# Kernel tuning notes

Measured on AMD Instinct MI355X. Metric: run time of the kernel, lower is better.

The kernel has to match this reference:

```python
import jax, jax.numpy as jnp
import numpy as np

# Model dims (mamba_ssm defaults: expand=2, d_state=16, d_conv=4, dt_rank=ceil(d_model/16))
V, D_MODEL, N_LAYERS = 32000, 768, 2
D_INNER, D_STATE, D_CONV, DT_RANK = 1536, 16, 4, 48
BATCH, SEQ = 2, 2048


def setup_inputs() -> dict:
    key = jax.random.key(0)
    ks = jax.random.split(key, 10)

    def nrm(k, shape, s=0.02):
        return (jax.random.normal(k, shape) * s).astype(jnp.float32)

    x = jax.random.randint(ks[0], (BATCH, SEQ), 0, V)
    emb = nrm(ks[1], (V, D_MODEL))
    # per-layer Mamba params, stacked on leading layer axis
    W_in = nrm(ks[2], (N_LAYERS, 2 * D_INNER, D_MODEL))          # in_proj (no bias)
    conv_w = nrm(ks[3], (N_LAYERS, D_INNER, 1, D_CONV), 0.1)      # depthwise causal conv
    conv_b = jnp.zeros((N_LAYERS, D_INNER), jnp.float32)
    W_x = nrm(ks[4], (N_LAYERS, DT_RANK + 2 * D_STATE, D_INNER))  # x_proj (no bias)
    W_dt = nrm(ks[5], (N_LAYERS, D_INNER, DT_RANK), 0.05)         # dt_proj
    b_dt = jnp.full((N_LAYERS, D_INNER), -4.0, jnp.float32)       # softplus(-4) ~ small dt
    # A initialized as -exp(A_log) with A_log = log(1..d_state), per mamba_ssm
    A_log = jnp.log(jnp.broadcast_to(
        jnp.arange(1, D_STATE + 1, dtype=jnp.float32), (N_LAYERS, D_INNER, D_STATE)))
    D_skip = jnp.ones((N_LAYERS, D_INNER), jnp.float32)
    W_out = nrm(ks[6], (N_LAYERS, D_MODEL, D_INNER))              # out_proj (no bias)
    ln_g = jnp.ones((D_MODEL,), jnp.float32)
    ln_b = jnp.zeros((D_MODEL,), jnp.float32)
    head_w = nrm(ks[7], (V, D_MODEL))
    head_b = jnp.zeros((V,), jnp.float32)
    return dict(x=x, emb=emb, W_in=W_in, conv_w=conv_w, conv_b=conv_b, W_x=W_x,
                W_dt=W_dt, b_dt=b_dt, A_log=A_log, D_skip=D_skip, W_out=W_out,
                ln_g=ln_g, ln_b=ln_b, head_w=head_w, head_b=head_b)


def mamba_block(h, W_in, conv_w, conv_b, W_x, W_dt, b_dt, A_log, D_skip, W_out):
    # h: (B, L, D_MODEL)
    xz = jnp.einsum('bld,ed->ble', h, W_in)              # (B, L, 2*d_inner)
    u, z = jnp.split(xz, 2, axis=-1)
    # causal depthwise conv over time
    uc = jnp.transpose(u, (0, 2, 1))                     # (B, d_inner, L)
    uc = jax.lax.conv_general_dilated(
        uc, conv_w, window_strides=(1,), padding=[(D_CONV - 1, 0)],
        feature_group_count=D_INNER, dimension_numbers=('NCH', 'OIH', 'NCH'))
    u = jax.nn.silu(jnp.transpose(uc, (0, 2, 1)) + conv_b)
    # input-dependent dt, B, C
    x_dbl = jnp.einsum('bld,ed->ble', u, W_x)            # (B, L, dt_rank+2*d_state)
    dtl, Bm, Cm = jnp.split(x_dbl, [DT_RANK, DT_RANK + D_STATE], axis=-1)
    dt = jax.nn.softplus(jnp.einsum('blr,dr->bld', dtl, W_dt) + b_dt)  # (B, L, d_inner)
    A = -jnp.exp(A_log)                                  # (d_inner, d_state)

    def step(hst, inp):
        dt_t, u_t, B_t, C_t = inp                        # (B,d_inner),(B,d_inner),(B,d_state),(B,d_state)
        hst = jnp.exp(dt_t[..., None] * A) * hst + (dt_t * u_t)[..., None] * B_t[:, None, :]
        y_t = jnp.einsum('bds,bs->bd', hst, C_t)
        return hst, y_t

    h0 = jnp.zeros((u.shape[0], D_INNER, D_STATE), u.dtype)
    xs = (dt.transpose(1, 0, 2), u.transpose(1, 0, 2),
          Bm.transpose(1, 0, 2), Cm.transpose(1, 0, 2))
    _, ys = jax.lax.scan(step, h0, xs)                   # (L, B, d_inner)
    y = ys.transpose(1, 0, 2) + u * D_skip
    y = y * jax.nn.silu(z)
    return jnp.einsum('bli,oi->blo', y, W_out)           # back to (B, L, D_MODEL)


def reference(x, emb, W_in, conv_w, conv_b, W_x, W_dt, b_dt, A_log, D_skip,
              W_out, ln_g, ln_b, head_w, head_b):
    h = emb[x]                                           # (B, L, D_MODEL)
    for l in range(N_LAYERS):
        h = h + mamba_block(h, W_in[l], conv_w[l], conv_b[l], W_x[l], W_dt[l],
                            b_dt[l], A_log[l], D_skip[l], W_out[l])
    mu = jnp.mean(h, axis=-1, keepdims=True)
    var = jnp.mean((h - mu) ** 2, axis=-1, keepdims=True)
    hn = (h - mu) * jax.lax.rsqrt(var + 1e-5) * ln_g + ln_b
    return jnp.einsum('bld,vd->blv', hn, head_w) + head_b
```

## Files before the change

kernel.cpp:

```cpp
#include <hip/hip_runtime.h>
#include <hip/hip_bf16.h>
#include <stdint.h>

#define BL    4096
#define DM    768
#define DI    1536
#define DS    16
#define DCONV 4
#define DTR   48
#define NL    2
#define SEQL  2048
#define BATCH 2
#define VOC   32000
#define NCH   32
#define CT    64

typedef __bf16 bf16_t;
typedef __bf16 bf16x8 __attribute__((ext_vector_type(8)));
typedef __bf16 bf16x4 __attribute__((ext_vector_type(4)));
typedef float  f32x4  __attribute__((ext_vector_type(4)));

__device__ __forceinline__ float sigmoidf_(float x) { return 1.f / (1.f + __expf(-x)); }
__device__ __forceinline__ float softplus_(float x) {
  return (x > 20.f) ? x : log1pf(__expf(x));
}

__global__ __launch_bounds__(256) void k_embed(const int* __restrict__ x,
                                               const float* __restrict__ emb,
                                               float* __restrict__ h,
                                               bf16_t* __restrict__ hb) {
  int row = blockIdx.x;
  int tok = x[row];
  const float* e = emb + (size_t)tok * DM;
  float* hr = h + (size_t)row * DM;
  bf16_t* hbr = hb + (size_t)row * DM;
  for (int c = threadIdx.x; c < DM; c += 256) {
    float v = e[c];
    hr[c] = v;
    hbr[c] = (bf16_t)v;
  }
}

#define NV0 1179648L
#define NV1 589824L
#define NV2 6144000L
#define NS3 393216L
#define NS4 196608L
#define NVT (NV0 + NV1 + NV2)
#define NTOT (NVT + NS3 + NS4)

__global__ __launch_bounds__(256) void k_cvtw(const float* __restrict__ Win,
                                              const float* __restrict__ Wout,
                                              const float* __restrict__ Whead,
                                              const float* __restrict__ Wx,
                                              const float* __restrict__ Wdt,
                                              bf16_t* __restrict__ bin,
                                              bf16_t* __restrict__ bout,
                                              bf16_t* __restrict__ bhead,
                                              bf16_t* __restrict__ bx,
                                              bf16_t* __restrict__ bdt) {
  long i = (long)blockIdx.x * 256 + threadIdx.x;
  if (i >= NTOT) return;
  if (i < NVT) {
    const float* s; bf16_t* d; long j = i;
    if (i < NV0)            { s = Win;   d = bin; }
    else if (i < NV0 + NV1) { s = Wout;  d = bout;  j = i - NV0; }
    else                    { s = Whead; d = bhead; j = i - NV0 - NV1; }
    float4 v = ((const float4*)s)[j];
    bf16x4 o;
    o[0] = (bf16_t)v.x; o[1] = (bf16_t)v.y; o[2] = (bf16_t)v.z; o[3] = (bf16_t)v.w;
    ((bf16x4*)d)[j] = o;
  } else if (i < NVT + NS3) {
    long j = i - NVT;
    int l = (int)(j / (128 * 1536));
    int rr = (int)((j / 1536) % 128);
    int c = (int)(j % 1536);
    bx[j] = (bf16_t)(rr < 80 ? Wx[((long)l * 80 + rr) * 1536 + c] : 0.f);
  } else {
    long j = i - NVT - NS3;
    int l = (int)(j / (1536 * 64));
    int r = (int)((j / 64) % 1536);
    int c = (int)(j & 63);
    bdt[j] = (bf16_t)(c < DTR ? Wdt[((long)l * 1536 + r) * DTR + c] : 0.f);
  }
}

__global__ __launch_bounds__(256) void k_cvt_pad(const float* __restrict__ src,
                                                 bf16_t* __restrict__ dst,
                                                 int R, int C, int srcLd, int Cpad,
                                                 long total) {
  long i = (long)blockIdx.x * 256 + threadIdx.x;
  if (i >= total) return;
  int r = (int)(i / Cpad), c = (int)(i % Cpad);
  float v = (r < R && c < C) ? src[(size_t)r * srcLd + c] : 0.f;
  dst[i] = (bf16_t)v;
}

__global__ __launch_bounds__(256) void k_zero(float* __restrict__ p, long n4) {
  long i = (long)blockIdx.x * 256 + threadIdx.x;
  if (i < n4) ((float4*)p)[i] = (float4){0.f, 0.f, 0.f, 0.f};
}

__global__ __launch_bounds__(256) void k_conv(const float* __restrict__ xz,
                                              const float* __restrict__ cw,
                                              const float* __restrict__ cb,
                                              bf16_t* __restrict__ ucb, long total) {
  long i = (long)blockIdx.x * 256 + threadIdx.x;
  if (i >= total) return;
  int d = (int)(i % DI);
  long row = i / DI;
  int l = (int)(row % SEQL);
  const float* w = cw + (size_t)d * DCONV;
  float s = cb[d];
#pragma unroll
  for (int j = 0; j < DCONV; j++) {
    int lj = l - (DCONV - 1) + j;
    if (lj >= 0) s += xz[(row - (DCONV - 1) + j) * (2 * DI) + d] * w[j];
  }
  float v = s * sigmoidf_(s);
  ucb[i] = (bf16_t)v;
}

__global__ __launch_bounds__(256) void k_scan1(const float* __restrict__ dt,
                                               const bf16_t* __restrict__ uc,
                                               const float* __restrict__ xdbl,
                                               const float* __restrict__ A_log,
                                               float* __restrict__ cA,
                                               float* __restrict__ cB) {
  int gi = blockIdx.x * 256 + threadIdx.x;
  int s = gi & 15;
  int rest = gi >> 4;
  int d = rest % DI;
  int rest2 = rest / DI;
  int c = rest2 % NCH;
  int b = rest2 / NCH;
  float a = -__expf(A_log[d * DS + s]);
  long l0 = (long)c * CT;
  const float*  dtp = dt + ((long)b * SEQL + l0) * DI + d;
  const bf16_t* ucp = uc + ((long)b * SEQL + l0) * DI + d;
  const float*  Bp  = xdbl + ((long)b * SEQL + l0) * 80 + DTR + s;
  float S = 0.f, hh = 0.f;
#pragma unroll 4
  for (int l = 0; l < CT; l++) {
    float dtv = dtp[(long)l * DI];
    float uv  = (float)ucp[(long)l * DI];
    float Bv  = Bp[(long)l * 80];
    S += dtv;
    hh = __expf(dtv * a) * hh + (dtv * uv) * Bv;
  }
  cA[gi] = __expf(a * S);
  cB[gi] = hh;
}

__global__ __launch_bounds__(256) void k_scan2(const float* __restrict__ cA,
                                               const float* __restrict__ cB,
                                               float* __restrict__ hst) {
  int gj = blockIdx.x * 256 + threadIdx.x;
  int ds_ = gj & (DI * DS - 1);
  int b = gj / (DI * DS);
  float h = 0.f;
#pragma unroll
  for (int c = 0; c < NCH; c++) {
    long idx = ((long)(b * NCH + c) * DI * DS) + ds_;
    hst[idx] = h;
    h = cA[idx] * h + cB[idx];
  }
}

__global__ __launch_bounds__(256) void k_scan3g(const float* __restrict__ dt,
                                                const bf16_t* uc,
                                                const float* __restrict__ xdbl,
                                                const float* __restrict__ A_log,
                                                const float* __restrict__ hst,
                                                const float* __restrict__ xz,
                                                const float* __restrict__ Dsk,
                                                bf16_t* o) {
  int gi = blockIdx.x * 256 + threadIdx.x;
  int s = gi & 15;
  int rest = gi >> 4;
  int d = rest % DI;
  int rest2 = rest / DI;
  int c = rest2 % NCH;
  int b = rest2 / NCH;
  float a = -__expf(A_log[d * DS + s]);
  float dval = Dsk[d];
  long l0 = (long)c * CT;
  const float*  dtp = dt + ((long)b * SEQL + l0) * DI + d;
  const bf16_t* ucp = uc + ((long)b * SEQL + l0) * DI + d;
  const float*  Bp  = xdbl + ((long)b * SEQL + l0) * 80 + DTR + s;
  const float*  Cp  = Bp + DS;
  const float*  zp  = xz + ((long)b * SEQL + l0) * (2 * DI) + DI + d;
  bf16_t* yp = o + ((long)b * SEQL + l0) * DI + d;
  float h = hst[gi];
#pragma unroll 4
  for (int l = 0; l < CT; l++) {
    float dtv = dtp[(long)l * DI];
    float uv  = (float)ucp[(long)l * DI];
    float Bv  = Bp[(long)l * 80];
    float Cv  = Cp[(long)l * 80];
    h = __expf(dtv * a) * h + (dtv * uv) * Bv;
    float y = h * Cv;
    y += __shfl_xor(y, 1);
    y += __shfl_xor(y, 2);
    y += __shfl_xor(y, 4);
    y += __shfl_xor(y, 8);
    if (s == 0) {
      float z = zp[(long)l * 2 * DI];
      float yy = (y + uv * dval) * z * sigmoidf_(z);
      yp[(long)l * DI] = (bf16_t)yy;
    }
  }
}

__global__ __launch_bounds__(256) void k_ln(const float* __restrict__ h,
                                            const float* __restrict__ g,
                                            const float* __restrict__ bta,
                                            bf16_t* __restrict__ o) {
  __shared__ float sm[4];
  int row = blockIdx.x;
  int t = threadIdx.x;
  const float* hr = h + (long)row * DM;
  float v0 = hr[t], v1 = hr[t + 256], v2 = hr[t + 512];
  float s = v0 + v1 + v2;
#pragma unroll
  for (int off = 32; off > 0; off >>= 1) s += __shfl_down(s, off);
  if ((t & 63) == 0) sm[t >> 6] = s;
  __syncthreads();
  float mu = (sm[0] + sm[1] + sm[2] + sm[3]) * (1.f / DM);
  __syncthreads();
  float d0 = v0 - mu, d1 = v1 - mu, d2 = v2 - mu;
  float q = d0 * d0 + d1 * d1 + d2 * d2;
#pragma unroll
  for (int off = 32; off > 0; off >>= 1) q += __shfl_down(q, off);
  if ((t & 63) == 0) sm[t >> 6] = q;
  __syncthreads();
  float var = (sm[0] + sm[1] + sm[2] + sm[3]) * (1.f / DM);
  float rs = rsqrtf(var + 1e-5f);
  bf16_t* orow = o + (long)row * DM;
  orow[t]       = (bf16_t)(d0 * rs * g[t]       + bta[t]);
  orow[t + 256] = (bf16_t)(d1 * rs * g[t + 256] + bta[t + 256]);
  orow[t + 512] = (bf16_t)(d2 * rs * g[t + 512] + bta[t + 512]);
}

__device__ __forceinline__ void stage16(const bf16_t* gp, bf16_t* lp) {
  __builtin_amdgcn_global_load_lds(
      (const __attribute__((address_space(1))) uint32_t*)gp,
      (__attribute__((address_space(3))) uint32_t*)lp, 16, 0, 0);
}


#define GLD128(ab, j, ktt, pp) do {                                             \
    int idx_ = (j) * 256 + tid;                                                 \
    int r_ = idx_ >> 3; int c16_ = idx_ & 7;                                    \
    size_t col_ = (size_t)(ktt) * 64 + (size_t)((c16_ ^ (r_ & 7)) << 3);        \
    const bf16_t* gp_ = (ab) ? (Wp + ((size_t)(n0 + r_)) * K + col_)            \
                             : (Ap + ((size_t)(m0 + r_)) * K + col_);           \
    bf16_t* lp_ = lds + ((((pp) * 2 + (ab)) * 128 + r_) * 64) + c16_ * 8;       \
    stage16(gp_, lp_);                                                          \
  } while (0)

#define STAGE8(pp, ktt) do {                                                    \
    GLD128(0, 0, ktt, pp); GLD128(0, 1, ktt, pp);                               \
    GLD128(0, 2, ktt, pp); GLD128(0, 3, ktt, pp);                               \
    GLD128(1, 0, ktt, pp); GLD128(1, 1, ktt, pp);                               \
    GLD128(1, 2, ktt, pp); GLD128(1, 3, ktt, pp);                               \
  } while (0)

#define COMPUTE128(pp, kh) do {                                                 \
    const char* lb_ = (const char*)lds;                                         \
    bf16x8 af_[4], bv_[4];                                                      \
    _Pragma("unroll") for (int f = 0; f < 4; ++f) {                             \
      int row_ = wm * 64 + f * 16 + fr;                                         \
      int byte_ = (((pp) * 2 + 0) * 128 + row_) * 128 +                         \
                  (((kh) * 64 + kq * 16) ^ ((row_ & 7) << 4));                  \
      af_[f] = *(const bf16x8*)(lb_ + byte_);                                   \
    }                                                                           \
    _Pragma("unroll") for (int f = 0; f < 4; ++f) {                             \
      int row_ = wn * 64 + f * 16 + fr;                                         \
      int byte_ = (((pp) * 2 + 1) * 128 + row_) * 128 +                         \
                  (((kh) * 64 + kq * 16) ^ ((row_ & 7) << 4));                  \
      bv_[f] = *(const bf16x8*)(lb_ + byte_);                                   \
    }                                                                           \
    __builtin_amdgcn_s_setprio(1);                                              \
    _Pragma("unroll") for (int fm = 0; fm < 4; ++fm)                            \
      _Pragma("unroll") for (int fn = 0; fn < 4; ++fn)                          \
        acc[fm][fn] = __builtin_amdgcn_mfma_f32_16x16x32_bf16(                  \
            af_[fm], bv_[fn], acc[fm][fn], 0, 0, 0);                            \
    __builtin_amdgcn_s_setprio(0);                                              \
  } while (0)

#define WAITV8()  asm volatile("s_waitcnt vmcnt(8)" ::: "memory")
#define WAITV0()  asm volatile("s_waitcnt vmcnt(0)" ::: "memory")
#define BARRIER() do { __builtin_amdgcn_s_barrier();                            \
                       asm volatile("" ::: "memory"); } while (0)

template <int EPI>
__global__ __launch_bounds__(256, 2) void k_gemm128(const bf16_t* __restrict__ Ap,
                                                    const bf16_t* __restrict__ Wp,
                                                    float* __restrict__ C,
                                                    const float* __restrict__ bias,
                                                    bf16_t* __restrict__ side,
                                                    int K, int ldc) {
  __shared__ bf16_t lds[2 * 2 * 128 * 64];
  const int tid = threadIdx.x;
  const int lane = tid & 63;
  const int wv = tid >> 6;
  const int wm = wv >> 1, wn = wv & 1;
  const int fr = lane & 15, kq = lane >> 4;

  const int cpx = gridDim.x >> 3;
  const int wg = ((int)blockIdx.x & 7) * cpx + ((int)blockIdx.x >> 3);
  const long m0 = (long)(wg & 31) * 128;
  const long n0 = (long)(wg >> 5) * 128;

  f32x4 acc[4][4];
#pragma unroll
  for (int i = 0; i < 4; i++)
#pragma unroll
    for (int j = 0; j < 4; j++) acc[i][j] = (f32x4){0.f, 0.f, 0.f, 0.f};

  STAGE8(0, 0);
  const int NT = K >> 6;
  for (int kt = 0; kt < NT; ++kt) {
    const int p = kt & 1;
    const bool pre = (kt + 1 < NT);
    if (pre) STAGE8(p ^ 1, kt + 1);
    if (pre) WAITV8(); else WAITV0();
    BARRIER();
    COMPUTE128(p, 0);
    COMPUTE128(p, 1);
    BARRIER();
  }

  {
    float* lf = (float*)(void*)lds;
    const int q = lane >> 4;
    const int cc = lane & 15;
    const int colt = (tid & 31) * 4;
    float4 bias4 = {0.f, 0.f, 0.f, 0.f};
    if (EPI == 1 || EPI == 3) bias4 = *(const float4*)&bias[n0 + colt];
#pragma unroll
    for (int p = 0; p < 4; ++p) {
      __syncthreads();
      if (wm == (p >> 1)) {
#pragma unroll
        for (int fl = 0; fl < 2; ++fl) {
          int fm = (p & 1) * 2 + fl;
#pragma unroll
          for (int fn = 0; fn < 4; ++fn) {
            f32x4 v = acc[fm][fn];
            float* dst = &lf[(fl * 16 + q * 4) * 128 + wn * 64 + fn * 16 + cc];
#pragma unroll
            for (int r = 0; r < 4; ++r) dst[r * 128] = v[r];
          }
        }
      }
      __syncthreads();
      const long rowg0 = m0 + p * 32;
#pragma unroll
      for (int it = 0; it < 4; ++it) {
        int rl = it * 8 + (tid >> 5);
        f32x4 v = *(const f32x4*)&lf[rl * 128 + colt];
        long row = rowg0 + rl;
        long cg = n0 + colt;
        float* gp = &C[row * (long)ldc + cg];
        if (EPI == 0) {
          *(f32x4*)gp = v;
        } else if (EPI == 1) {
          v[0] += bias4.x; v[1] += bias4.y; v[2] += bias4.z; v[3] += bias4.w;
          __builtin_nontemporal_store(v, (f32x4*)gp);
        } else if (EPI == 3) {
          v[0] = softplus_(v[0] + bias4.x);
          v[1] = softplus_(v[1] + bias4.y);
          v[2] = softplus_(v[2] + bias4.z);
          v[3] = softplus_(v[3] + bias4.w);
          *(f32x4*)gp = v;
        } else {
          f32x4 c0 = *(const f32x4*)gp;
          v[0] += c0[0]; v[1] += c0[1]; v[2] += c0[2]; v[3] += c0[3];
          *(f32x4*)gp = v;
          bf16x4 s4;
          s4[0] = (bf16_t)v[0]; s4[1] = (bf16_t)v[1];
          s4[2] = (bf16_t)v[2]; s4[3] = (bf16_t)v[3];
          *(bf16x4*)&side[row * (long)ldc + cg] = s4;
        }
      }
    }
  }
}

__global__ __launch_bounds__(256) void k_gemm_sk(const bf16_t* __restrict__ A,
                                                 const bf16_t* __restrict__ W,
                                                 float* __restrict__ C,
                                                 int N, int K, int KS, int ldc) {
  __shared__ bf16_t lA[128 * 32];
  __shared__ bf16_t lB[128 * 32];
  const int tid = threadIdx.x;
  const int lane = tid & 63;
  const int wv = tid >> 6;
  const int wm = wv >> 1, wn = wv & 1;
  const long m0 = (long)blockIdx.y * 128;
  const long n0 = (long)blockIdx.x * 128;
  const int kLo = blockIdx.z * KS;
  const int r0 = tid >> 2;
  const int c8 = (tid & 3) * 8;
  const int fr = lane & 15;
  const int kq = lane >> 4;

  f32x4 acc[4][4];
#pragma unroll
  for (int i = 0; i < 4; i++)
#pragma unroll
    for (int j = 0; j < 4; j++) acc[i][j] = (f32x4){0.f, 0.f, 0.f, 0.f};

  const bf16_t* Ab = A + (m0 + r0) * (long)K + c8;
  const bf16_t* Wb = W + (n0 + r0) * (long)K + c8;
  bf16_t* lAp = lA + r0 * 32 + c8;
  bf16_t* lBp = lB + r0 * 32 + c8;
  const long s64K = 64L * K;

  for (int k0 = kLo; k0 < kLo + KS; k0 += 32) {
    __syncthreads();
    stage16(Ab + k0, lAp);
    stage16(Ab + k0 + s64K, lAp + 64 * 32);
    stage16(Wb + k0, lBp);
    stage16(Wb + k0 + s64K, lBp + 64 * 32);
    __syncthreads();
    bf16x8 af[4], bfv[4];
#pragma unroll
    for (int f = 0; f < 4; f++)
      af[f] = *(const bf16x8*)&lA[(wm * 64 + f * 16 + fr) * 32 + kq * 8];
#pragma unroll
    for (int f = 0; f < 4; f++)
      bfv[f] = *(const bf16x8*)&lB[(wn * 64 + f * 16 + fr) * 32 + kq * 8];
#pragma unroll
    for (int fm = 0; fm < 4; fm++)
#pragma unroll
      for (int fn = 0; fn < 4; fn++)
        acc[fm][fn] = __builtin_amdgcn_mfma_f32_16x16x32_bf16(af[fm], bfv[fn],
                                                              acc[fm][fn], 0, 0, 0);
  }

  const int r4 = (lane >> 4) * 4;
  const int cc = lane & 15;
#pragma unroll
  for (int fm = 0; fm < 4; fm++) {
    long rowb = m0 + wm * 64 + fm * 16 + r4;
#pragma unroll
    for (int fn = 0; fn < 4; fn++) {
      long col = n0 + wn * 64 + fn * 16 + cc;
      if (col < N) {
#pragma unroll
        for (int r = 0; r < 4; r++)
          atomicAdd(&C[(rowb + r) * (long)ldc + col], acc[fm][fn][r]);
      }
    }
  }
}

static inline int cdiv_l(long a, long b) { return (int)((a + b - 1) / b); }

extern "C" void kernel_launch(void* const* d_in, const int* in_sizes, int n_in,
                              void* d_out, int out_size, void* d_ws, size_t ws_size,
                              hipStream_t stream) {
  (void)in_sizes; (void)n_in; (void)out_size; (void)ws_size;
  const int*   x      = (const int*)  d_in[0];
  const float* emb    = (const float*)d_in[1];
  const float* W_in   = (const float*)d_in[2];
  const float* conv_w = (const float*)d_in[3];
  const float* conv_b = (const float*)d_in[4];
  const float* W_x    = (const float*)d_in[5];
  const float* W_dt   = (const float*)d_in[6];
  const float* b_dt   = (const float*)d_in[7];
  const float* A_log  = (const float*)d_in[8];
  const float* D_skip = (const float*)d_in[9];
  const float* W_out  = (const float*)d_in[10];
  const float* ln_g   = (const float*)d_in[11];
  const float* ln_b   = (const float*)d_in[12];
  const float* head_w = (const float*)d_in[13];
  const float* head_b = (const float*)d_in[14];
  float* out = (float*)d_out;

  bf16_t* abuf   = (bf16_t*)d_ws;
  bf16_t* hbf    = abuf   + (size_t)BL * DI;
  bf16_t* dtl    = hbf    + (size_t)BL * DM;
  bf16_t* wb_in  = dtl    + (size_t)BL * 64;
  bf16_t* wb_out = wb_in  + (size_t)2 * 3072 * 768;
  bf16_t* wb_hd  = wb_out + (size_t)2 * 768 * 1536;
  bf16_t* wb_x   = wb_hd  + (size_t)VOC * DM;
  bf16_t* wb_dt  = wb_x   + (size_t)2 * 128 * 1536;

  float* xz   = out;
  float* xdbl = xz   + (size_t)BL * 2 * DI;
  float* dtb  = xdbl + (size_t)BL * 80;
  float* h    = dtb  + (size_t)BL * DI;
  float* cA   = h    + (size_t)BL * DM;
  float* cB   = cA   + (size_t)BATCH * NCH * DI * DS;
  float* hst  = cB   + (size_t)BATCH * NCH * DI * DS;

  const int scan_blocks = BATCH * NCH * DI * DS / 256;
  const int st_blocks   = BATCH * DI * DS / 256;

  k_cvtw<<<cdiv_l(NTOT, 256), 256, 0, stream>>>(W_in, W_out, head_w, W_x, W_dt,
                                                wb_in, wb_out, wb_hd, wb_x, wb_dt);
  k_embed<<<BL, 256, 0, stream>>>(x, emb, h, hbf);

  for (int l = 0; l < NL; ++l) {
    k_gemm128<0><<<(BL / 128) * (2 * DI / 128), 256, 0, stream>>>(
        hbf, wb_in + (size_t)l * 3072 * 768, xz, nullptr, nullptr, DM, 2 * DI);
    k_conv<<<cdiv_l((long)BL * DI, 256), 256, 0, stream>>>(
        xz, conv_w + (size_t)l * DI * DCONV, conv_b + (size_t)l * DI,
        abuf, (long)BL * DI);
    k_zero<<<cdiv_l((long)BL * 80 / 4, 256), 256, 0, stream>>>(xdbl, (long)BL * 80 / 4);
    k_gemm_sk<<<dim3(1, BL / 128, 4), 256, 0, stream>>>(
        abuf, wb_x + (size_t)l * 128 * 1536, xdbl, 80, DI, DI / 4, 80);
    k_cvt_pad<<<cdiv_l((long)BL * 64, 256), 256, 0, stream>>>(
        xdbl, dtl, BL, DTR, 80, 64, (long)BL * 64);
    k_gemm128<3><<<(BL / 128) * (DI / 128), 256, 0, stream>>>(
        dtl, wb_dt + (size_t)l * 1536 * 64, dtb, b_dt + (size_t)l * DI, nullptr,
        64, DI);
    k_scan1<<<scan_blocks, 256, 0, stream>>>(dtb, abuf, xdbl,
                                             A_log + (size_t)l * DI * DS, cA, cB);
    k_scan2<<<st_blocks, 256, 0, stream>>>(cA, cB, hst);
    k_scan3g<<<scan_blocks, 256, 0, stream>>>(dtb, abuf, xdbl,
                                              A_log + (size_t)l * DI * DS, hst,
                                              xz, D_skip + (size_t)l * DI, abuf);
    k_gemm128<5><<<(BL / 128) * (DM / 128), 256, 0, stream>>>(
        abuf, wb_out + (size_t)l * 768 * 1536, h, nullptr, hbf, DI, DM);
  }

  k_ln<<<BL, 256, 0, stream>>>(h, ln_g, ln_b, abuf);
  k_gemm128<1><<<(BL / 128) * (VOC / 128), 256, 0, stream>>>(
      abuf, wb_hd, out, head_b, nullptr, DM, VOC);
}
```

Before: 1.072 ms.

## Add 256x256 GEMM kernel for in_proj and LM head, unify split-K x_proj

Adds a 512-thread GEMM kernel with 256x256 output tiles, used for the in_proj and the large vocabulary head GEMMs, so each loaded tile is reused across more MFMAs and per-block overhead drops. The separate split-K x_proj kernel is removed; that GEMM now runs through the double-buffered 128 kernel with a K-slice offset and an atomic epilogue. Epilogue LDS strides are padded to cut bank conflicts. The larger tile raises register and LDS use and may lower occupancy. It also leaves fewer blocks in flight for the smaller GEMMs.

```diff
diff --git a/kernel.cpp b/kernel.cpp
--- a/kernel.cpp
+++ b/kernel.cpp
@@ -248,18 +248,143 @@
       (__attribute__((address_space(3))) uint32_t*)lp, 16, 0, 0);
 }
 
+#define WAITV8()  asm volatile("s_waitcnt vmcnt(8)" ::: "memory")
+#define WAITV0()  asm volatile("s_waitcnt vmcnt(0)" ::: "memory")
+#define BARRIER() do { __builtin_amdgcn_s_barrier();                            \
+                       asm volatile("" ::: "memory"); } while (0)
+
+
+#define GLD256(ab, j, ktt, pp) do {                                             \
+    int idx_ = (j) * 512 + tid;                                                 \
+    int r_ = idx_ >> 3; int c16_ = idx_ & 7;                                    \
+    size_t col_ = (size_t)(ktt) * 64 + (size_t)((c16_ ^ (r_ & 7)) << 3);        \
+    const bf16_t* gp_ = (ab) ? (Wp + ((size_t)(n0 + r_)) * K + col_)            \
+                             : (Ap + ((size_t)(m0 + r_)) * K + col_);           \
+    bf16_t* lp_ = lds + ((((pp) * 2 + (ab)) * 256 + r_) * 64) + c16_ * 8;       \
+    stage16(gp_, lp_);                                                          \
+  } while (0)
+
+#define STAGE256(pp, ktt) do {                                                  \
+    GLD256(0, 0, ktt, pp); GLD256(0, 1, ktt, pp);                               \
+    GLD256(0, 2, ktt, pp); GLD256(0, 3, ktt, pp);                               \
+    GLD256(1, 0, ktt, pp); GLD256(1, 1, ktt, pp);                               \
+    GLD256(1, 2, ktt, pp); GLD256(1, 3, ktt, pp);                               \
+  } while (0)
+
+#define COMPUTE_KH(pp, kh) do {                                                 \
+    const char* lb_ = (const char*)lds;                                         \
+    bf16x8 bfr_[4];                                                             \
+    _Pragma("unroll") for (int f = 0; f < 4; ++f) {                             \
+      int row_ = wn * 64 + f * 16 + fr;                                         \
+      int byte_ = (((pp) * 2 + 1) * 256 + row_) * 128 +                         \
+                  (((kh) * 64 + kq * 16) ^ ((row_ & 7) << 4));                  \
+      bfr_[f] = *(const bf16x8*)(lb_ + byte_);                                  \
+    }                                                                           \
+    _Pragma("unroll") for (int mg = 0; mg < 2; ++mg) {                          \
+      bf16x8 afr_[4];                                                           \
+      _Pragma("unroll") for (int f = 0; f < 4; ++f) {                           \
+        int row_ = wm * 128 + mg * 64 + f * 16 + fr;                            \
+        int byte_ = (((pp) * 2 + 0) * 256 + row_) * 128 +                       \
+                    (((kh) * 64 + kq * 16) ^ ((row_ & 7) << 4));                \
+        afr_[f] = *(const bf16x8*)(lb_ + byte_);                                \
+      }                                                                         \
+      __builtin_amdgcn_s_setprio(1);                                            \
+      _Pragma("unroll") for (int fm = 0; fm < 4; ++fm)                          \
+        _Pragma("unroll") for (int fn = 0; fn < 4; ++fn)                        \
+          acc[mg * 4 + fm][fn] = __builtin_amdgcn_mfma_f32_16x16x32_bf16(       \
+              afr_[fm], bfr_[fn], acc[mg * 4 + fm][fn], 0, 0, 0);               \
+      __builtin_amdgcn_s_setprio(0);                                            \
+    }                                                                           \
+  } while (0)
+
+template <int EPI>
+__global__ __launch_bounds__(512, 2) void k_gemm256(const bf16_t* __restrict__ Ap,
+                                                    const bf16_t* __restrict__ Wp,
+                                                    float* __restrict__ C,
+                                                    const float* __restrict__ bias,
+                                                    int K, int ldc) {
+  __shared__ bf16_t lds[2 * 2 * 256 * 64];
+  const int tid = threadIdx.x;
+  const int lane = tid & 63;
+  const int wid = tid >> 6;
+  const int wm = wid >> 2, wn = wid & 3;
+  const int fr = lane & 15, kq = lane >> 4;
+
+  const int cpx = gridDim.x >> 3;
+  const int wg = ((int)blockIdx.x & 7) * cpx + ((int)blockIdx.x >> 3);
+  const long m0 = (long)(wg & 15) * 256;
+  const long n0 = (long)(wg >> 4) * 256;
+
+  f32x4 acc[8][4];
+#pragma unroll
+  for (int i = 0; i < 8; i++)
+#pragma unroll
+    for (int j = 0; j < 4; j++) acc[i][j] = (f32x4){0.f, 0.f, 0.f, 0.f};
+
+  STAGE256(0, 0);
+  const int NT = K >> 6;
+  for (int kt = 0; kt < NT; ++kt) {
+    const int p = kt & 1;
+    const bool pre = (kt + 1 < NT);
+    if (pre) STAGE256(p ^ 1, kt + 1);
+    if (pre) WAITV8(); else WAITV0();
+    BARRIER();
+    COMPUTE_KH(p, 0);
+    COMPUTE_KH(p, 1);
+    BARRIER();
+  }
+
+  {
+    float* lf = (float*)(void*)lds;
+    const int q = lane >> 4;
+    const int cc = lane & 15;
+    float4 bias4 = {0.f, 0.f, 0.f, 0.f};
+    if (EPI == 1) bias4 = *(const float4*)&bias[n0 + lane * 4];
+#pragma unroll
+    for (int p = 0; p < 4; ++p) {
+      __syncthreads();
+      if (wm == (p >> 1)) {
+        const int mgb = (p & 1) * 4;
+#pragma unroll
+        for (int m4 = 0; m4 < 4; ++m4)
+#pragma unroll
+          for (int n = 0; n < 4; ++n) {
+            f32x4 v = acc[mgb + m4][n];
+            float* dst = &lf[(m4 * 16 + q * 4) * 260 + wn * 64 + n * 16 + cc];
+#pragma unroll
+            for (int r = 0; r < 4; ++r) dst[r * 260] = v[r];
+          }
+      }
+      __syncthreads();
+      const long rowg0 = m0 + p * 64;
+#pragma unroll
+      for (int it = 0; it < 8; ++it) {
+        int row_loc = wid * 8 + it;
+        f32x4 v = *(const f32x4*)&lf[row_loc * 260 + lane * 4];
+        float* gp = &C[(rowg0 + row_loc) * (long)ldc + n0 + lane * 4];
+        if (EPI == 1) {
+          v[0] += bias4.x; v[1] += bias4.y; v[2] += bias4.z; v[3] += bias4.w;
+          __builtin_nontemporal_store(v, (f32x4*)gp);
+        } else {
+          *(f32x4*)gp = v;
+        }
+      }
+    }
+  }
+}
+
 
 #define GLD128(ab, j, ktt, pp) do {                                             \
     int idx_ = (j) * 256 + tid;                                                 \
     int r_ = idx_ >> 3; int c16_ = idx_ & 7;                                    \
-    size_t col_ = (size_t)(ktt) * 64 + (size_t)((c16_ ^ (r_ & 7)) << 3);        \
+    size_t col_ = kb + (size_t)(ktt) * 64 + (size_t)((c16_ ^ (r_ & 7)) << 3);   \
     const bf16_t* gp_ = (ab) ? (Wp + ((size_t)(n0 + r_)) * K + col_)            \
                              : (Ap + ((size_t)(m0 + r_)) * K + col_);           \
     bf16_t* lp_ = lds + ((((pp) * 2 + (ab)) * 128 + r_) * 64) + c16_ * 8;       \
     stage16(gp_, lp_);                                                          \
   } while (0)
 
-#define STAGE8(pp, ktt) do {                                                    \
+#define STAGE128(pp, ktt) do {                                                  \
     GLD128(0, 0, ktt, pp); GLD128(0, 1, ktt, pp);                               \
     GLD128(0, 2, ktt, pp); GLD128(0, 3, ktt, pp);                               \
     GLD128(1, 0, ktt, pp); GLD128(1, 1, ktt, pp);                               \
@@ -270,16 +395,16 @@
     const char* lb_ = (const char*)lds;                                         \
     bf16x8 af_[4], bv_[4];                                                      \
     _Pragma("unroll") for (int f = 0; f < 4; ++f) {                             \
+      int row_ = wn * 64 + f * 16 + fr;                                         \
+      int byte_ = (((pp) * 2 + 1) * 128 + row_) * 128 +                         \
+                  (((kh) * 64 + kq * 16) ^ ((row_ & 7) << 4));                  \
+      bv_[f] = *(const bf16x8*)(lb_ + byte_);                                   \
+    }                                                                           \
+    _Pragma("unroll") for (int f = 0; f < 4; ++f) {                             \
       int row_ = wm * 64 + f * 16 + fr;                                         \
       int byte_ = (((pp) * 2 + 0) * 128 + row_) * 128 +                         \
                   (((kh) * 64 + kq * 16) ^ ((row_ & 7) << 4));                  \
       af_[f] = *(const bf16x8*)(lb_ + byte_);                                   \
-    }                                                                           \
-    _Pragma("unroll") for (int f = 0; f < 4; ++f) {                             \
-      int row_ = wn * 64 + f * 16 + fr;                                         \
-      int byte_ = (((pp) * 2 + 1) * 128 + row_) * 128 +                         \
-                  (((kh) * 64 + kq * 16) ^ ((row_ & 7) << 4));                  \
-      bv_[f] = *(const bf16x8*)(lb_ + byte_);                                   \
     }                                                                           \
     __builtin_amdgcn_s_setprio(1);                                              \
     _Pragma("unroll") for (int fm = 0; fm < 4; ++fm)                            \
@@ -289,24 +414,20 @@
     __builtin_amdgcn_s_setprio(0);                                              \
   } while (0)
 
-#define WAITV8()  asm volatile("s_waitcnt vmcnt(8)" ::: "memory")
-#define WAITV0()  asm volatile("s_waitcnt vmcnt(0)" ::: "memory")
-#define BARRIER() do { __builtin_amdgcn_s_barrier();                            \
-                       asm volatile("" ::: "memory"); } while (0)
-
 template <int EPI>
 __global__ __launch_bounds__(256, 2) void k_gemm128(const bf16_t* __restrict__ Ap,
                                                     const bf16_t* __restrict__ Wp,
                                                     float* __restrict__ C,
                                                     const float* __restrict__ bias,
                                                     bf16_t* __restrict__ side,
-                                                    int K, int ldc) {
+                                                    int K, int Ksl, int ldc) {
   __shared__ bf16_t lds[2 * 2 * 128 * 64];
   const int tid = threadIdx.x;
   const int lane = tid & 63;
   const int wv = tid >> 6;
   const int wm = wv >> 1, wn = wv & 1;
   const int fr = lane & 15, kq = lane >> 4;
+  const size_t kb = (size_t)blockIdx.y * Ksl;
 
   const int cpx = gridDim.x >> 3;
   const int wg = ((int)blockIdx.x & 7) * cpx + ((int)blockIdx.x >> 3);
@@ -319,17 +440,36 @@
 #pragma unroll
     for (int j = 0; j < 4; j++) acc[i][j] = (f32x4){0.f, 0.f, 0.f, 0.f};
 
-  STAGE8(0, 0);
-  const int NT = K >> 6;
+  STAGE128(0, 0);
+  const int NT = Ksl >> 6;
   for (int kt = 0; kt < NT; ++kt) {
     const int p = kt & 1;
     const bool pre = (kt + 1 < NT);
-    if (pre) STAGE8(p ^ 1, kt + 1);
+    if (pre) STAGE128(p ^ 1, kt + 1);
     if (pre) WAITV8(); else WAITV0();
     BARRIER();
     COMPUTE128(p, 0);
     COMPUTE128(p, 1);
     BARRIER();
+  }
+
+  if (EPI == 6) {
+    const int r4 = (lane >> 4) * 4;
+    const int cc = lane & 15;
+#pragma unroll
+    for (int fm = 0; fm < 4; fm++) {
+      long rowb = m0 + wm * 64 + fm * 16 + r4;
+#pragma unroll
+      for (int fn = 0; fn < 4; fn++) {
+        long col = n0 + wn * 64 + fn * 16 + cc;
+        if (col < 80) {
+#pragma unroll
+          for (int r = 0; r < 4; r++)
+            atomicAdd(&C[(rowb + r) * (long)ldc + col], acc[fm][fn][r]);
+        }
+      }
+    }
+    return;
   }
 
   {
@@ -338,7 +478,7 @@
     const int cc = lane & 15;
     const int colt = (tid & 31) * 4;
     float4 bias4 = {0.f, 0.f, 0.f, 0.f};
-    if (EPI == 1 || EPI == 3) bias4 = *(const float4*)&bias[n0 + colt];
+    if (EPI == 3) bias4 = *(const float4*)&bias[n0 + colt];
 #pragma unroll
     for (int p = 0; p < 4; ++p) {
       __syncthreads();
@@ -349,9 +489,9 @@
 #pragma unroll
           for (int fn = 0; fn < 4; ++fn) {
             f32x4 v = acc[fm][fn];
-            float* dst = &lf[(fl * 16 + q * 4) * 128 + wn * 64 + fn * 16 + cc];
-#pragma unroll
-            for (int r = 0; r < 4; ++r) dst[r * 128] = v[r];
+            float* dst = &lf[(fl * 16 + q * 4) * 132 + wn * 64 + fn * 16 + cc];
+#pragma unroll
+            for (int r = 0; r < 4; ++r) dst[r * 132] = v[r];
           }
         }
       }
@@ -360,16 +500,11 @@
 #pragma unroll
       for (int it = 0; it < 4; ++it) {
         int rl = it * 8 + (tid >> 5);
-        f32x4 v = *(const f32x4*)&lf[rl * 128 + colt];
+        f32x4 v = *(const f32x4*)&lf[rl * 132 + colt];
         long row = rowg0 + rl;
         long cg = n0 + colt;
         float* gp = &C[row * (long)ldc + cg];
-        if (EPI == 0) {
-          *(f32x4*)gp = v;
-        } else if (EPI == 1) {
-          v[0] += bias4.x; v[1] += bias4.y; v[2] += bias4.z; v[3] += bias4.w;
-          __builtin_nontemporal_store(v, (f32x4*)gp);
-        } else if (EPI == 3) {
+        if (EPI == 3) {
           v[0] = softplus_(v[0] + bias4.x);
           v[1] = softplus_(v[1] + bias4.y);
           v[2] = softplus_(v[2] + bias4.z);
@@ -384,75 +519,6 @@
           s4[2] = (bf16_t)v[2]; s4[3] = (bf16_t)v[3];
           *(bf16x4*)&side[row * (long)ldc + cg] = s4;
         }
-      }
-    }
-  }
-}
-
-__global__ __launch_bounds__(256) void k_gemm_sk(const bf16_t* __restrict__ A,
-                                                 const bf16_t* __restrict__ W,
-                                                 float* __restrict__ C,
-                                                 int N, int K, int KS, int ldc) {
-  __shared__ bf16_t lA[128 * 32];
-  __shared__ bf16_t lB[128 * 32];
-  const int tid = threadIdx.x;
-  const int lane = tid & 63;
-  const int wv = tid >> 6;
-  const int wm = wv >> 1, wn = wv & 1;
-  const long m0 = (long)blockIdx.y * 128;
-  const long n0 = (long)blockIdx.x * 128;
-  const int kLo = blockIdx.z * KS;
-  const int r0 = tid >> 2;
-  const int c8 = (tid & 3) * 8;
-  const int fr = lane & 15;
-  const int kq = lane >> 4;
-
-  f32x4 acc[4][4];
-#pragma unroll
-  for (int i = 0; i < 4; i++)
-#pragma unroll
-    for (int j = 0; j < 4; j++) acc[i][j] = (f32x4){0.f, 0.f, 0.f, 0.f};
-
-  const bf16_t* Ab = A + (m0 + r0) * (long)K + c8;
-  const bf16_t* Wb = W + (n0 + r0) * (long)K + c8;
-  bf16_t* lAp = lA + r0 * 32 + c8;
-  bf16_t* lBp = lB + r0 * 32 + c8;
-  const long s64K = 64L * K;
-
-  for (int k0 = kLo; k0 < kLo + KS; k0 += 32) {
-    __syncthreads();
-    stage16(Ab + k0, lAp);
-    stage16(Ab + k0 + s64K, lAp + 64 * 32);
-    stage16(Wb + k0, lBp);
-    stage16(Wb + k0 + s64K, lBp + 64 * 32);
-    __syncthreads();
-    bf16x8 af[4], bfv[4];
-#pragma unroll
-    for (int f = 0; f < 4; f++)
-      af[f] = *(const bf16x8*)&lA[(wm * 64 + f * 16 + fr) * 32 + kq * 8];
-#pragma unroll
-    for (int f = 0; f < 4; f++)
-      bfv[f] = *(const bf16x8*)&lB[(wn * 64 + f * 16 + fr) * 32 + kq * 8];
-#pragma unroll
-    for (int fm = 0; fm < 4; fm++)
-#pragma unroll
-      for (int fn = 0; fn < 4; fn++)
-        acc[fm][fn] = __builtin_amdgcn_mfma_f32_16x16x32_bf16(af[fm], bfv[fn],
-                                                              acc[fm][fn], 0, 0, 0);
-  }
-
-  const int r4 = (lane >> 4) * 4;
-  const int cc = lane & 15;
-#pragma unroll
-  for (int fm = 0; fm < 4; fm++) {
-    long rowb = m0 + wm * 64 + fm * 16 + r4;
-#pragma unroll
-    for (int fn = 0; fn < 4; fn++) {
-      long col = n0 + wn * 64 + fn * 16 + cc;
-      if (col < N) {
-#pragma unroll
-        for (int r = 0; r < 4; r++)
-          atomicAdd(&C[(rowb + r) * (long)ldc + col], acc[fm][fn][r]);
       }
     }
   }
@@ -506,19 +572,20 @@
   k_embed<<<BL, 256, 0, stream>>>(x, emb, h, hbf);
 
   for (int l = 0; l < NL; ++l) {
-    k_gemm128<0><<<(BL / 128) * (2 * DI / 128), 256, 0, stream>>>(
-        hbf, wb_in + (size_t)l * 3072 * 768, xz, nullptr, nullptr, DM, 2 * DI);
+    k_gemm256<0><<<(BL / 256) * (2 * DI / 256), 512, 0, stream>>>(
+        hbf, wb_in + (size_t)l * 3072 * 768, xz, nullptr, DM, 2 * DI);
     k_conv<<<cdiv_l((long)BL * DI, 256), 256, 0, stream>>>(
         xz, conv_w + (size_t)l * DI * DCONV, conv_b + (size_t)l * DI,
         abuf, (long)BL * DI);
     k_zero<<<cdiv_l((long)BL * 80 / 4, 256), 256, 0, stream>>>(xdbl, (long)BL * 80 / 4);
-    k_gemm_sk<<<dim3(1, BL / 128, 4), 256, 0, stream>>>(
-        abuf, wb_x + (size_t)l * 128 * 1536, xdbl, 80, DI, DI / 4, 80);
+    k_gemm128<6><<<dim3(32, 4), 256, 0, stream>>>(
+        abuf, wb_x + (size_t)l * 128 * 1536, xdbl, nullptr, nullptr,
+        DI, DI / 4, 80);
     k_cvt_pad<<<cdiv_l((long)BL * 64, 256), 256, 0, stream>>>(
         xdbl, dtl, BL, DTR, 80, 64, (long)BL * 64);
     k_gemm128<3><<<(BL / 128) * (DI / 128), 256, 0, stream>>>(
         dtl, wb_dt + (size_t)l * 1536 * 64, dtb, b_dt + (size_t)l * DI, nullptr,
-        64, DI);
+        64, 64, DI);
     k_scan1<<<scan_blocks, 256, 0, stream>>>(dtb, abuf, xdbl,
                                              A_log + (size_t)l * DI * DS, cA, cB);
     k_scan2<<<st_blocks, 256, 0, stream>>>(cA, cB, hst);
@@ -526,10 +593,10 @@
                                               A_log + (size_t)l * DI * DS, hst,
                                               xz, D_skip + (size_t)l * DI, abuf);
     k_gemm128<5><<<(BL / 128) * (DM / 128), 256, 0, stream>>>(
-        abuf, wb_out + (size_t)l * 768 * 1536, h, nullptr, hbf, DI, DM);
+        abuf, wb_out + (size_t)l * 768 * 1536, h, nullptr, hbf, DI, DI, DM);
   }
 
   k_ln<<<BL, 256, 0, stream>>>(h, ln_g, ln_b, abuf);
-  k_gemm128<1><<<(BL / 128) * (VOC / 128), 256, 0, stream>>>(
-      abuf, wb_hd, out, head_b, nullptr, DM, VOC);
-}
+  k_gemm256<1><<<(BL / 256) * (VOC / 256), 512, 0, stream>>>(
+      abuf, wb_hd, out, head_b, DM, VOC);
+}
```

Result: faster. 988.4 us (-7.8%).

## Shrink GEMM K-tile to 32, add split-K epilogue, fuse zeroing into conv

Applied to the files above, without the earlier changes.

Reworks the main GEMM kernel to stage 32-wide K tiles with a new swizzled LDS layout. This halves shared memory per block so occupancy can go from 2 to 3 blocks per CU. The same kernel gains a split-K atomic epilogue that replaces the separate x_proj GEMM, and the zeroing of xdbl is folded into the conv kernel to drop a launch. The epilogue staging stride is padded from 128 to 132 to avoid LDS bank conflicts. The smaller K tile means more barriers per FLOP, and the deeper split-K adds more atomic traffic.

```diff
diff --git a/kernel.cpp b/kernel.cpp
--- a/kernel.cpp
+++ b/kernel.cpp
@@ -96,16 +96,13 @@
   dst[i] = (bf16_t)v;
 }
 
-__global__ __launch_bounds__(256) void k_zero(float* __restrict__ p, long n4) {
-  long i = (long)blockIdx.x * 256 + threadIdx.x;
-  if (i < n4) ((float4*)p)[i] = (float4){0.f, 0.f, 0.f, 0.f};
-}
-
 __global__ __launch_bounds__(256) void k_conv(const float* __restrict__ xz,
                                               const float* __restrict__ cw,
                                               const float* __restrict__ cb,
-                                              bf16_t* __restrict__ ucb, long total) {
+                                              bf16_t* __restrict__ ucb, long total,
+                                              float* __restrict__ zbuf, long nz4) {
   long i = (long)blockIdx.x * 256 + threadIdx.x;
+  if (i < nz4) ((float4*)zbuf)[i] = (float4){0.f, 0.f, 0.f, 0.f};
   if (i >= total) return;
   int d = (int)(i % DI);
   long row = i / DI;
@@ -248,65 +245,67 @@
       (__attribute__((address_space(3))) uint32_t*)lp, 16, 0, 0);
 }
 
-
-#define GLD128(ab, j, ktt, pp) do {                                             \
-    int idx_ = (j) * 256 + tid;                                                 \
-    int r_ = idx_ >> 3; int c16_ = idx_ & 7;                                    \
-    size_t col_ = (size_t)(ktt) * 64 + (size_t)((c16_ ^ (r_ & 7)) << 3);        \
+#define WAITV4()  asm volatile("s_waitcnt vmcnt(4)" ::: "memory")
+#define WAITV0()  asm volatile("s_waitcnt vmcnt(0)" ::: "memory")
+#define BARRIER() do { __builtin_amdgcn_s_barrier();                            \
+                       asm volatile("" ::: "memory"); } while (0)
+
+
+#define GLD32(ab, j, ktt, pp) do {                                              \
+    int L_ = (j) * 4096 + tid * 16;                                             \
+    int rowp_ = L_ >> 7;                                                        \
+    int chs_ = (L_ >> 4) & 7;                                                   \
+    int chl_ = chs_ ^ (rowp_ & 7);                                              \
+    int r_ = rowp_ * 2 + (chl_ >> 2);                                           \
+    size_t col_ = kb + (size_t)(ktt) * 32 + (size_t)((chl_ & 3) * 8);           \
     const bf16_t* gp_ = (ab) ? (Wp + ((size_t)(n0 + r_)) * K + col_)            \
                              : (Ap + ((size_t)(m0 + r_)) * K + col_);           \
-    bf16_t* lp_ = lds + ((((pp) * 2 + (ab)) * 128 + r_) * 64) + c16_ * 8;       \
+    bf16_t* lp_ = lds + ((((pp) * 2 + (ab)) * 64 + rowp_) * 64) + chs_ * 8;     \
     stage16(gp_, lp_);                                                          \
   } while (0)
 
-#define STAGE8(pp, ktt) do {                                                    \
-    GLD128(0, 0, ktt, pp); GLD128(0, 1, ktt, pp);                               \
-    GLD128(0, 2, ktt, pp); GLD128(0, 3, ktt, pp);                               \
-    GLD128(1, 0, ktt, pp); GLD128(1, 1, ktt, pp);                               \
-    GLD128(1, 2, ktt, pp); GLD128(1, 3, ktt, pp);                               \
+#define STAGE4(pp, ktt) do {                                                    \
+    GLD32(0, 0, ktt, pp); GLD32(0, 1, ktt, pp);                                 \
+    GLD32(1, 0, ktt, pp); GLD32(1, 1, ktt, pp);                                 \
   } while (0)
 
-#define COMPUTE128(pp, kh) do {                                                 \
+#define FRAG_BYTE(ab, pp, row_)                                                 \
+    ((((pp) * 2 + (ab)) * 64 + ((row_) >> 1)) * 128 +                           \
+     (((((row_) & 1) * 4 + kq) ^ (((row_) >> 1) & 7)) * 16))
+
+#define COMPUTE32(pp) do {                                                      \
     const char* lb_ = (const char*)lds;                                         \
-    bf16x8 af_[4], bv_[4];                                                      \
+    bf16x8 bv_[4], av_[4];                                                      \
+    _Pragma("unroll") for (int f = 0; f < 4; ++f) {                             \
+      int row_ = wn * 64 + f * 16 + fr;                                         \
+      bv_[f] = *(const bf16x8*)(lb_ + FRAG_BYTE(1, pp, row_));                  \
+    }                                                                           \
     _Pragma("unroll") for (int f = 0; f < 4; ++f) {                             \
       int row_ = wm * 64 + f * 16 + fr;                                         \
-      int byte_ = (((pp) * 2 + 0) * 128 + row_) * 128 +                         \
-                  (((kh) * 64 + kq * 16) ^ ((row_ & 7) << 4));                  \
-      af_[f] = *(const bf16x8*)(lb_ + byte_);                                   \
-    }                                                                           \
-    _Pragma("unroll") for (int f = 0; f < 4; ++f) {                             \
-      int row_ = wn * 64 + f * 16 + fr;                                         \
-      int byte_ = (((pp) * 2 + 1) * 128 + row_) * 128 +                         \
-                  (((kh) * 64 + kq * 16) ^ ((row_ & 7) << 4));                  \
-      bv_[f] = *(const bf16x8*)(lb_ + byte_);                                   \
+      av_[f] = *(const bf16x8*)(lb_ + FRAG_BYTE(0, pp, row_));                  \
     }                                                                           \
     __builtin_amdgcn_s_setprio(1);                                              \
     _Pragma("unroll") for (int fm = 0; fm < 4; ++fm)                            \
       _Pragma("unroll") for (int fn = 0; fn < 4; ++fn)                          \
         acc[fm][fn] = __builtin_amdgcn_mfma_f32_16x16x32_bf16(                  \
-            af_[fm], bv_[fn], acc[fm][fn], 0, 0, 0);                            \
+            av_[fm], bv_[fn], acc[fm][fn], 0, 0, 0);                            \
     __builtin_amdgcn_s_setprio(0);                                              \
   } while (0)
 
-#define WAITV8()  asm volatile("s_waitcnt vmcnt(8)" ::: "memory")
-#define WAITV0()  asm volatile("s_waitcnt vmcnt(0)" ::: "memory")
-#define BARRIER() do { __builtin_amdgcn_s_barrier();                            \
-                       asm volatile("" ::: "memory"); } while (0)
-
 template <int EPI>
-__global__ __launch_bounds__(256, 2) void k_gemm128(const bf16_t* __restrict__ Ap,
-                                                    const bf16_t* __restrict__ Wp,
-                                                    float* __restrict__ C,
-                                                    const float* __restrict__ bias,
-                                                    bf16_t* __restrict__ side,
-                                                    int K, int ldc) {
-  __shared__ bf16_t lds[2 * 2 * 128 * 64];
+__global__ __launch_bounds__(256, 3) void k_gemm(const bf16_t* __restrict__ Ap,
+                                                 const bf16_t* __restrict__ Wp,
+                                                 float* __restrict__ C,
+                                                 const float* __restrict__ bias,
+                                                 bf16_t* __restrict__ side,
+                                                 int K, int Ksl, int ldc) {
+  __shared__ bf16_t lds[2 * 2 * 64 * 64];
   const int tid = threadIdx.x;
   const int lane = tid & 63;
   const int wv = tid >> 6;
   const int wm = wv >> 1, wn = wv & 1;
   const int fr = lane & 15, kq = lane >> 4;
+  const size_t kb = (size_t)blockIdx.y * Ksl;
 
   const int cpx = gridDim.x >> 3;
   const int wg = ((int)blockIdx.x & 7) * cpx + ((int)blockIdx.x >> 3);
@@ -319,17 +318,35 @@
 #pragma unroll
     for (int j = 0; j < 4; j++) acc[i][j] = (f32x4){0.f, 0.f, 0.f, 0.f};
 
-  STAGE8(0, 0);
-  const int NT = K >> 6;
+  STAGE4(0, 0);
+  const int NT = Ksl >> 5;
   for (int kt = 0; kt < NT; ++kt) {
     const int p = kt & 1;
     const bool pre = (kt + 1 < NT);
-    if (pre) STAGE8(p ^ 1, kt + 1);
-    if (pre) WAITV8(); else WAITV0();
+    if (pre) STAGE4(p ^ 1, kt + 1);
+    if (pre) WAITV4(); else WAITV0();
     BARRIER();
-    COMPUTE128(p, 0);
-    COMPUTE128(p, 1);
+    COMPUTE32(p);
     BARRIER();
+  }
+
+  if (EPI == 6) {
+    const int r4 = (lane >> 4) * 4;
+    const int cc = lane & 15;
+#pragma unroll
+    for (int fm = 0; fm < 4; fm++) {
+      long rowb = m0 + wm * 64 + fm * 16 + r4;
+#pragma unroll
+      for (int fn = 0; fn < 4; fn++) {
+        long col = n0 + wn * 64 + fn * 16 + cc;
+        if (col < 80) {
+#pragma unroll
+          for (int r = 0; r < 4; r++)
+            atomicAdd(&C[(rowb + r) * (long)ldc + col], acc[fm][fn][r]);
+        }
+      }
+    }
+    return;
   }
 
   {
@@ -349,9 +366,9 @@
 #pragma unroll
           for (int fn = 0; fn < 4; ++fn) {
             f32x4 v = acc[fm][fn];
-            float* dst = &lf[(fl * 16 + q * 4) * 128 + wn * 64 + fn * 16 + cc];
-#pragma unroll
-            for (int r = 0; r < 4; ++r) dst[r * 128] = v[r];
+            float* dst = &lf[(fl * 16 + q * 4) * 132 + wn * 64 + fn * 16 + cc];
+#pragma unroll
+            for (int r = 0; r < 4; ++r) dst[r * 132] = v[r];
           }
         }
       }
@@ -360,7 +377,7 @@
 #pragma unroll
       for (int it = 0; it < 4; ++it) {
         int rl = it * 8 + (tid >> 5);
-        f32x4 v = *(const f32x4*)&lf[rl * 128 + colt];
+        f32x4 v = *(const f32x4*)&lf[rl * 132 + colt];
         long row = rowg0 + rl;
         long cg = n0 + colt;
         float* gp = &C[row * (long)ldc + cg];
@@ -389,75 +406,6 @@
   }
 }
 
-__global__ __launch_bounds__(256) void k_gemm_sk(const bf16_t* __restrict__ A,
-                                                 const bf16_t* __restrict__ W,
-                                                 float* __restrict__ C,
-                                                 int N, int K, int KS, int ldc) {
-  __shared__ bf16_t lA[128 * 32];
-  __shared__ bf16_t lB[128 * 32];
-  const int tid = threadIdx.x;
-  const int lane = tid & 63;
-  const int wv = tid >> 6;
-  const int wm = wv >> 1, wn = wv & 1;
-  const long m0 = (long)blockIdx.y * 128;
-  const long n0 = (long)blockIdx.x * 128;
-  const int kLo = blockIdx.z * KS;
-  const int r0 = tid >> 2;
-  const int c8 = (tid & 3) * 8;
-  const int fr = lane & 15;
-  const int kq = lane >> 4;
-
-  f32x4 acc[4][4];
-#pragma unroll
-  for (int i = 0; i < 4; i++)
-#pragma unroll
-    for (int j = 0; j < 4; j++) acc[i][j] = (f32x4){0.f, 0.f, 0.f, 0.f};
-
-  const bf16_t* Ab = A + (m0 + r0) * (long)K + c8;
-  const bf16_t* Wb = W + (n0 + r0) * (long)K + c8;
-  bf16_t* lAp = lA + r0 * 32 + c8;
-  bf16_t* lBp = lB + r0 * 32 + c8;
-  const long s64K = 64L * K;
-
-  for (int k0 = kLo; k0 < kLo + KS; k0 += 32) {
-    __syncthreads();
-    stage16(Ab + k0, lAp);
-    stage16(Ab + k0 + s64K, lAp + 64 * 32);
-    stage16(Wb + k0, lBp);
-    stage16(Wb + k0 + s64K, lBp + 64 * 32);
-    __syncthreads();
-    bf16x8 af[4], bfv[4];
-#pragma unroll
-    for (int f = 0; f < 4; f++)
-      af[f] = *(const bf16x8*)&lA[(wm * 64 + f * 16 + fr) * 32 + kq * 8];
-#pragma unroll
-    for (int f = 0; f < 4; f++)
-      bfv[f] = *(const bf16x8*)&lB[(wn * 64 + f * 16 + fr) * 32 + kq * 8];
-#pragma unroll
-    for (int fm = 0; fm < 4; fm++)
-#pragma unroll
-      for (int fn = 0; fn < 4; fn++)
-        acc[fm][fn] = __builtin_amdgcn_mfma_f32_16x16x32_bf16(af[fm], bfv[fn],
-                                                              acc[fm][fn], 0, 0, 0);
-  }
-
-  const int r4 = (lane >> 4) * 4;
-  const int cc = lane & 15;
-#pragma unroll
-  for (int fm = 0; fm < 4; fm++) {
-    long rowb = m0 + wm * 64 + fm * 16 + r4;
-#pragma unroll
-    for (int fn = 0; fn < 4; fn++) {
-      long col = n0 + wn * 64 + fn * 16 + cc;
-      if (col < N) {
-#pragma unroll
-        for (int r = 0; r < 4; r++)
-          atomicAdd(&C[(rowb + r) * (long)ldc + col], acc[fm][fn][r]);
-      }
-    }
-  }
-}
-
 static inline int cdiv_l(long a, long b) { return (int)((a + b - 1) / b); }
 
 extern "C" void kernel_launch(void* const* d_in, const int* in_sizes, int n_in,
@@ -506,30 +454,31 @@
   k_embed<<<BL, 256, 0, stream>>>(x, emb, h, hbf);
 
   for (int l = 0; l < NL; ++l) {
-    k_gemm128<0><<<(BL / 128) * (2 * DI / 128), 256, 0, stream>>>(
-        hbf, wb_in + (size_t)l * 3072 * 768, xz, nullptr, nullptr, DM, 2 * DI);
+    k_gemm<0><<<(BL / 128) * (2 * DI / 128), 256, 0, stream>>>(
+        hbf, wb_in + (size_t)l * 3072 * 768, xz, nullptr, nullptr,
+        DM, DM, 2 * DI);
     k_conv<<<cdiv_l((long)BL * DI, 256), 256, 0, stream>>>(
         xz, conv_w + (size_t)l * DI * DCONV, conv_b + (size_t)l * DI,
-        abuf, (long)BL * DI);
-    k_zero<<<cdiv_l((long)BL * 80 / 4, 256), 256, 0, stream>>>(xdbl, (long)BL * 80 / 4);
-    k_gemm_sk<<<dim3(1, BL / 128, 4), 256, 0, stream>>>(
-        abuf, wb_x + (size_t)l * 128 * 1536, xdbl, 80, DI, DI / 4, 80);
+        abuf, (long)BL * DI, xdbl, (long)BL * 80 / 4);
+    k_gemm<6><<<dim3(32, 8), 256, 0, stream>>>(
+        abuf, wb_x + (size_t)l * 128 * 1536, xdbl, nullptr, nullptr,
+        DI, DI / 8, 80);
     k_cvt_pad<<<cdiv_l((long)BL * 64, 256), 256, 0, stream>>>(
         xdbl, dtl, BL, DTR, 80, 64, (long)BL * 64);
-    k_gemm128<3><<<(BL / 128) * (DI / 128), 256, 0, stream>>>(
+    k_gemm<3><<<(BL / 128) * (DI / 128), 256, 0, stream>>>(
         dtl, wb_dt + (size_t)l * 1536 * 64, dtb, b_dt + (size_t)l * DI, nullptr,
-        64, DI);
+        64, 64, DI);
     k_scan1<<<scan_blocks, 256, 0, stream>>>(dtb, abuf, xdbl,
                                              A_log + (size_t)l * DI * DS, cA, cB);
     k_scan2<<<st_blocks, 256, 0, stream>>>(cA, cB, hst);
     k_scan3g<<<scan_blocks, 256, 0, stream>>>(dtb, abuf, xdbl,
                                               A_log + (size_t)l * DI * DS, hst,
                                               xz, D_skip + (size_t)l * DI, abuf);
-    k_gemm128<5><<<(BL / 128) * (DM / 128), 256, 0, stream>>>(
-        abuf, wb_out + (size_t)l * 768 * 1536, h, nullptr, hbf, DI, DM);
+    k_gemm<5><<<(BL / 128) * (DM / 128), 256, 0, stream>>>(
+        abuf, wb_out + (size_t)l * 768 * 1536, h, nullptr, hbf, DI, DI, DM);
   }
 
   k_ln<<<BL, 256, 0, stream>>>(h, ln_g, ln_b, abuf);
-  k_gemm128<1><<<(BL / 128) * (VOC / 128), 256, 0, stream>>>(
-      abuf, wb_hd, out, head_b, nullptr, DM, VOC);
-}
+  k_gemm<1><<<(BL / 128) * (VOC / 128), 256, 0, stream>>>(
+      abuf, wb_hd, out, head_b, nullptr, DM, DM, VOC);
+}
```

Result: no change. 1.069 ms (-0.3%).
